# Kernel tuning notes

Measured on AMD Instinct MI355X. Metric: run time of the kernel, lower is better.

Reference implementation:

```python
import jax, jax.numpy as jnp
import numpy as np

N_NODES = 100000
N_EDGES = 1600000
F_IN, NH1, NH2, NH3, N_CLS = 128, 64, 18, 9, 10
KS = [8, 6, 4, 4]
BN_EPS = 1e-5


def setup_inputs() -> dict:
    key = jax.random.key(0)
    ks = jax.random.split(key, 32)
    inp = {
        "x": jax.random.normal(ks[0], (N_NODES, F_IN), dtype=jnp.float32),
        "edge_index": jax.random.randint(ks[1], (2, N_EDGES), 0, N_NODES, dtype=jnp.int32),
    }
    dims = [(F_IN, NH1), (NH1, NH2), (NH2, NH3), (NH3, N_CLS)]
    for i, ((din, dout), K) in enumerate(zip(dims, KS), start=1):
        scale = 1.0 / np.sqrt(din * K)
        inp[f"W{i}"] = jax.random.normal(ks[2 * i], (K, din, dout), dtype=jnp.float32) * scale
        inp[f"b{i}"] = jnp.zeros((dout,), dtype=jnp.float32)
    for i, d in enumerate([NH1, NH2, NH3], start=1):
        inp[f"bn{i}_g"] = jnp.ones((d,), dtype=jnp.float32)
        inp[f"bn{i}_b"] = jnp.zeros((d,), dtype=jnp.float32)
        inp[f"bn{i}_m"] = jnp.zeros((d,), dtype=jnp.float32)
        inp[f"bn{i}_v"] = jnp.ones((d,), dtype=jnp.float32)
    return inp


def _cheb_conv(x, W, b, src, dst, w_norm, n_nodes):
    # PyG ChebConv with lambda_max=2: L_hat = -D^{-1/2} A D^{-1/2}
    def prop(t):  # L_hat @ t via edge scatter
        return jax.ops.segment_sum(w_norm[:, None] * t[src], dst, num_segments=n_nodes)

    K = W.shape[0]
    Tx0 = x
    out = Tx0 @ W[0]
    Tx1 = prop(Tx0)
    out = out + Tx1 @ W[1]
    for k in range(2, K):
        Tx2 = 2.0 * prop(Tx1) - Tx0
        out = out + Tx2 @ W[k]
        Tx0, Tx1 = Tx1, Tx2
    return out + b


def _bn_eval(x, g, b, m, v):
    return (x - m) * (g * jax.lax.rsqrt(v + BN_EPS)) + b


def reference(x, edge_index, W1, b1, W2, b2, W3, b3, W4, b4,
              bn1_g, bn1_b, bn1_m, bn1_v,
              bn2_g, bn2_b, bn2_m, bn2_v,
              bn3_g, bn3_b, bn3_m, bn3_v):
    n = x.shape[0]
    src, dst = edge_index[0], edge_index[1]
    ones = jnp.ones((src.shape[0],), dtype=x.dtype)
    deg = jax.ops.segment_sum(ones, dst, num_segments=n)
    dinv = jnp.where(deg > 0, jax.lax.rsqrt(jnp.maximum(deg, 1.0)), 0.0)
    w_norm = -dinv[src] * dinv[dst]

    h = jax.nn.relu(_bn_eval(_cheb_conv(x, W1, b1, src, dst, w_norm, n), bn1_g, bn1_b, bn1_m, bn1_v))
    h = jax.nn.relu(_bn_eval(_cheb_conv(h, W2, b2, src, dst, w_norm, n), bn2_g, bn2_b, bn2_m, bn2_v))
    h = jax.nn.relu(_bn_eval(_cheb_conv(h, W3, b3, src, dst, w_norm, n), bn3_g, bn3_b, bn3_m, bn3_v))
    return _cheb_conv(h, W4, b4, src, dst, w_norm, n)
```

## Files before the change

kernel.cpp:

```cpp
#include <hip/hip_runtime.h>

#define NN 100000
#define NE 1600000
#define BN_EPS 1e-5f

#define BSH 7
#define BSZ (1 << BSH)
#define NBUCK 782
#define NC 192
#define CE 8334

typedef _Float16 half1;
typedef _Float16 half4 __attribute__((ext_vector_type(4)));
typedef _Float16 h8 __attribute__((ext_vector_type(8)));
typedef float f4 __attribute__((ext_vector_type(4)));
typedef float f8 __attribute__((ext_vector_type(8)));

static inline int divup(int a, int b) { return (a + b - 1) / b; }

__device__ __forceinline__ float wsrc(unsigned int q) {
    unsigned int dg = q >> 17;
    return dg ? rsqrtf((float)dg) : 0.f;
}


__global__ void histb_kernel(const int* __restrict__ dst, int* __restrict__ hist_g) {
    __shared__ int h[NBUCK];
    int c = blockIdx.x;
    for (int i = threadIdx.x; i < NBUCK; i += blockDim.x) h[i] = 0;
    __syncthreads();
    int e0 = c * CE, e1 = min(e0 + CE, NE);
    for (int e = e0 + threadIdx.x; e < e1; e += blockDim.x)
        atomicAdd(&h[dst[e] >> BSH], 1);
    __syncthreads();
    for (int i = threadIdx.x; i < NBUCK; i += blockDim.x) hist_g[c * NBUCK + i] = h[i];
}

__global__ void bscan1_kernel(const int* __restrict__ hist_g, int* __restrict__ bucket_start,
                              int* __restrict__ row_ptr) {
    __shared__ int sh[1024];
    int t = threadIdx.x;
    int tot = 0;
    if (t < NBUCK)
        for (int c = 0; c < NC; ++c) tot += hist_g[c * NBUCK + t];
    sh[t] = (t < NBUCK) ? tot : 0;
    __syncthreads();
    for (int off = 1; off < 1024; off <<= 1) {
        int v = (t >= off) ? sh[t - off] : 0;
        __syncthreads();
        sh[t] += v;
        __syncthreads();
    }
    if (t < NBUCK) bucket_start[t] = sh[t] - tot;
    if (t == 0) { bucket_start[NBUCK] = NE; row_ptr[NN] = NE; }
}

__global__ void boff_kernel(const int* __restrict__ bucket_start, const int* __restrict__ hist_g,
                            int* __restrict__ off_g) {
    int b = blockIdx.x * blockDim.x + threadIdx.x;
    if (b >= NBUCK) return;
    int run = bucket_start[b];
#pragma unroll 4
    for (int c = 0; c < NC; ++c) {
        off_g[c * NBUCK + b] = run;
        run += hist_g[c * NBUCK + b];
    }
}

__global__ void binscatter_kernel(const int* __restrict__ src, const int* __restrict__ dst,
                                  const int* __restrict__ off_g, unsigned int* __restrict__ tmp) {
    __shared__ int off_l[NBUCK];
    int myx = blockIdx.x & 7;
    int c = blockIdx.x >> 3;
    for (int i = threadIdx.x; i < NBUCK; i += blockDim.x)
        off_l[i] = ((i & 7) == myx) ? off_g[c * NBUCK + i] : 0;
    __syncthreads();
    int e0 = c * CE, e1 = min(e0 + CE, NE);
    for (int e = e0 + threadIdx.x; e < e1; e += blockDim.x) {
        int d = dst[e];
        int b = d >> BSH;
        if ((b & 7) != myx) continue;
        int s = src[e];
        int pos = atomicAdd(&off_l[b], 1);
        tmp[pos] = (unsigned int)s | ((unsigned int)(d & (BSZ - 1)) << 25);
    }
}

__global__ void finalize_kernel(const unsigned int* __restrict__ tmp,
                                const int* __restrict__ bucket_start,
                                int* __restrict__ row_ptr, int* __restrict__ deg,
                                unsigned int* __restrict__ cw) {
    __shared__ int cnt[BSZ], sc[BSZ], cur[BSZ];
    int b = blockIdx.x, t = threadIdx.x;
    int e0 = bucket_start[b], e1 = bucket_start[b + 1];
    if (t < BSZ) cnt[t] = 0;
    __syncthreads();
    for (int e = e0 + t; e < e1; e += blockDim.x) atomicAdd(&cnt[tmp[e] >> 25], 1);
    __syncthreads();
    if (t < BSZ) sc[t] = cnt[t];
    __syncthreads();
    for (int off = 1; off < BSZ; off <<= 1) {
        int v = (t >= off && t < BSZ) ? sc[t - off] : 0;
        __syncthreads();
        if (t < BSZ) sc[t] += v;
        __syncthreads();
    }
    if (t < BSZ) {
        int p = e0 + sc[t] - cnt[t];
        cur[t] = p;
        int nd = (b << BSH) + t;
        if (nd < NN) { row_ptr[nd] = p; deg[nd] = cnt[t]; }
    }
    __syncthreads();
    for (int e = e0 + t; e < e1; e += blockDim.x) {
        unsigned int r = tmp[e];
        int ld = r >> 25;
        int k = atomicAdd(&cur[ld], 1);
        cw[k] = r & 0x1FFFFu;
    }
}

__global__ void packdeg_kernel(unsigned int* __restrict__ cw, const int* __restrict__ deg) {
    int e = blockIdx.x * blockDim.x + threadIdx.x;
    if (e >= NE) return;
    unsigned int q = cw[e];
    int dg = deg[q];
    if (dg > 32767) dg = 32767;
    cw[e] = q | ((unsigned int)dg << 17);
}


__global__ void cvtx_kernel(const float4* __restrict__ X, half4* __restrict__ Xh, int tot4) {
    int i = blockIdx.x * blockDim.x + threadIdx.x;
    if (i >= tot4) return;
    float4 v = X[i];
    half4 h;
    h.x = (half1)v.x; h.y = (half1)v.y; h.z = (half1)v.z; h.w = (half1)v.w;
    Xh[i] = h;
}

__global__ void transw_kernel(const float* __restrict__ W, half1* __restrict__ Wt) {
    int i = blockIdx.x * blockDim.x + threadIdx.x;
    if (i >= 512 * 128) return;
    int kd = i >> 9;
    int og = i & 511;
    int k = og >> 6, o = og & 63;
    Wt[(size_t)og * 128 + kd] = (half1)W[((size_t)k * 128 + kd) * 64 + o];
}

__global__ void padw_kernel(const float* __restrict__ src, float* __restrict__ dst,
                            int K, int dins, int douts, int dind, int doutd) {
    int i = blockIdx.x * blockDim.x + threadIdx.x;
    int tot = K * dind * doutd;
    if (i >= tot) return;
    int o = i % doutd;
    int r = i / doutd;
    int dd = r % dind;
    int k = r / dind;
    dst[i] = (dd < dins && o < douts) ? src[((size_t)k * dins + dd) * douts + o] : 0.f;
}

__global__ void proph8_kernel(const h8* __restrict__ feat, const h8* __restrict__ sub,
                              const h8* __restrict__ add, h8* __restrict__ outh,
                              f8* __restrict__ outf,
                              const int* __restrict__ row_ptr, const unsigned int* __restrict__ cw,
                              int n, float scale, int has_sub, int bnrelu,
                              const float* __restrict__ bn_g, const float* __restrict__ bn_b,
                              const float* __restrict__ bn_m, const float* __restrict__ bn_v) {
    int idx = blockIdx.x * blockDim.x + threadIdx.x;
    if (idx >= n * 8) return;
    int nd = idx >> 3;
    int f = idx & 7;
    int e0 = row_ptr[nd], e1 = row_ptr[nd + 1];
    f8 a0 = {0.f, 0.f, 0.f, 0.f, 0.f, 0.f, 0.f, 0.f}, a1 = a0, a2 = a0, a3 = a0;
    int e = e0;
    for (; e + 8 <= e1; e += 8) {
        unsigned int q0 = cw[e], q1 = cw[e + 1], q2 = cw[e + 2], q3 = cw[e + 3];
        unsigned int q4 = cw[e + 4], q5 = cw[e + 5], q6 = cw[e + 6], q7 = cw[e + 7];
        f8 v0 = __builtin_convertvector(feat[(size_t)(q0 & 0x1FFFFu) * 8 + f], f8);
        f8 v1 = __builtin_convertvector(feat[(size_t)(q1 & 0x1FFFFu) * 8 + f], f8);
        f8 v2 = __builtin_convertvector(feat[(size_t)(q2 & 0x1FFFFu) * 8 + f], f8);
        f8 v3 = __builtin_convertvector(feat[(size_t)(q3 & 0x1FFFFu) * 8 + f], f8);
        f8 v4 = __builtin_convertvector(feat[(size_t)(q4 & 0x1FFFFu) * 8 + f], f8);
        f8 v5 = __builtin_convertvector(feat[(size_t)(q5 & 0x1FFFFu) * 8 + f], f8);
        f8 v6 = __builtin_convertvector(feat[(size_t)(q6 & 0x1FFFFu) * 8 + f], f8);
        f8 v7 = __builtin_convertvector(feat[(size_t)(q7 & 0x1FFFFu) * 8 + f], f8);
        a0 += wsrc(q0) * v0;
        a1 += wsrc(q1) * v1;
        a2 += wsrc(q2) * v2;
        a3 += wsrc(q3) * v3;
        a0 += wsrc(q4) * v4;
        a1 += wsrc(q5) * v5;
        a2 += wsrc(q6) * v6;
        a3 += wsrc(q7) * v7;
    }
    for (; e + 4 <= e1; e += 4) {
        unsigned int q0 = cw[e], q1 = cw[e + 1], q2 = cw[e + 2], q3 = cw[e + 3];
        f8 v0 = __builtin_convertvector(feat[(size_t)(q0 & 0x1FFFFu) * 8 + f], f8);
        f8 v1 = __builtin_convertvector(feat[(size_t)(q1 & 0x1FFFFu) * 8 + f], f8);
        f8 v2 = __builtin_convertvector(feat[(size_t)(q2 & 0x1FFFFu) * 8 + f], f8);
        f8 v3 = __builtin_convertvector(feat[(size_t)(q3 & 0x1FFFFu) * 8 + f], f8);
        a0 += wsrc(q0) * v0;
        a1 += wsrc(q1) * v1;
        a2 += wsrc(q2) * v2;
        a3 += wsrc(q3) * v3;
    }
    for (; e < e1; ++e) {
        unsigned int q = cw[e];
        a0 += wsrc(q) * __builtin_convertvector(feat[(size_t)(q & 0x1FFFFu) * 8 + f], f8);
    }
    int degd = e1 - e0;
    float ms = (degd > 0) ? -scale * rsqrtf((float)degd) : 0.f;
    f8 r = ((a0 + a1) + (a2 + a3)) * ms;
    if (has_sub) r -= __builtin_convertvector(sub[idx], f8);
    r += __builtin_convertvector(__builtin_nontemporal_load(&add[idx]), f8);
    if (bnrelu) {
#pragma unroll
        for (int c = 0; c < 8; ++c) {
            int o = f * 8 + c;
            float sc = bn_g[o] * rsqrtf(bn_v[o] + BN_EPS);
            r[c] = fmaxf(fmaf(r[c] - bn_m[o], sc, bn_b[o]), 0.f);
        }
    }
    if (outf) {
        outf[idx] = r;
    } else {
        outh[idx] = __builtin_convertvector(r, h8);
    }
}

__global__ void proph_kernel(const half4* __restrict__ feat, const half4* __restrict__ sub,
                             const half4* __restrict__ add, half4* __restrict__ outh,
                             f4* __restrict__ outf,
                             const int* __restrict__ row_ptr, const unsigned int* __restrict__ cw,
                             int n, int dim4, float scale, int has_sub,
                             int bnrelu, int used,
                             const float* __restrict__ bn_g, const float* __restrict__ bn_b,
                             const float* __restrict__ bn_m, const float* __restrict__ bn_v) {
    int idx = blockIdx.x * blockDim.x + threadIdx.x;
    if (idx >= n * dim4) return;
    int nd = idx / dim4;
    int f = idx - nd * dim4;
    int e0 = row_ptr[nd], e1 = row_ptr[nd + 1];
    f4 a0 = {0.f, 0.f, 0.f, 0.f}, a1 = a0, a2 = a0, a3 = a0;
    int e = e0;
    for (; e + 4 <= e1; e += 4) {
        unsigned int q0 = cw[e], q1 = cw[e + 1], q2 = cw[e + 2], q3 = cw[e + 3];
        f4 v0 = __builtin_convertvector(feat[(size_t)(q0 & 0x1FFFFu) * dim4 + f], f4);
        f4 v1 = __builtin_convertvector(feat[(size_t)(q1 & 0x1FFFFu) * dim4 + f], f4);
        f4 v2 = __builtin_convertvector(feat[(size_t)(q2 & 0x1FFFFu) * dim4 + f], f4);
        f4 v3 = __builtin_convertvector(feat[(size_t)(q3 & 0x1FFFFu) * dim4 + f], f4);
        a0 += wsrc(q0) * v0;
        a1 += wsrc(q1) * v1;
        a2 += wsrc(q2) * v2;
        a3 += wsrc(q3) * v3;
    }
    for (; e < e1; ++e) {
        unsigned int q = cw[e];
        a0 += wsrc(q) * __builtin_convertvector(feat[(size_t)(q & 0x1FFFFu) * dim4 + f], f4);
    }
    int degd = e1 - e0;
    float ms = (degd > 0) ? -scale * rsqrtf((float)degd) : 0.f;
    f4 r = ((a0 + a1) + (a2 + a3)) * ms;
    if (has_sub) r -= __builtin_convertvector(sub[idx], f4);
    r += __builtin_convertvector(__builtin_nontemporal_load(&add[idx]), f4);
    if (bnrelu) {
#pragma unroll
        for (int c = 0; c < 4; ++c) {
            int o = f * 4 + c;
            if (o < used) {
                float sc = bn_g[o] * rsqrtf(bn_v[o] + BN_EPS);
                r[c] = fmaxf(fmaf(r[c] - bn_m[o], sc, bn_b[o]), 0.f);
            } else r[c] = 0.f;
        }
    }
    if (outf) {
        outf[idx] = r;
    } else {
        half4 h;
        h.x = (half1)r.x; h.y = (half1)r.y; h.z = (half1)r.z; h.w = (half1)r.w;
        outh[idx] = h;
    }
}

__global__ void propl_kernel(const half4* __restrict__ feat, const half4* __restrict__ sub,
                             const half4* __restrict__ add, float* __restrict__ out,
                             const int* __restrict__ row_ptr, const unsigned int* __restrict__ cw,
                             int n) {
    int idx = blockIdx.x * blockDim.x + threadIdx.x;
    if (idx >= n * 3) return;
    int nd = idx / 3;
    int f = idx - nd * 3;
    int e0 = row_ptr[nd], e1 = row_ptr[nd + 1];
    f4 a0 = {0.f, 0.f, 0.f, 0.f}, a1 = a0, a2 = a0, a3 = a0;
    int e = e0;
    for (; e + 4 <= e1; e += 4) {
        unsigned int q0 = cw[e], q1 = cw[e + 1], q2 = cw[e + 2], q3 = cw[e + 3];
        a0 += wsrc(q0) * __builtin_convertvector(feat[(size_t)(q0 & 0x1FFFFu) * 3 + f], f4);
        a1 += wsrc(q1) * __builtin_convertvector(feat[(size_t)(q1 & 0x1FFFFu) * 3 + f], f4);
        a2 += wsrc(q2) * __builtin_convertvector(feat[(size_t)(q2 & 0x1FFFFu) * 3 + f], f4);
        a3 += wsrc(q3) * __builtin_convertvector(feat[(size_t)(q3 & 0x1FFFFu) * 3 + f], f4);
    }
    for (; e < e1; ++e) {
        unsigned int q = cw[e];
        a0 += wsrc(q) * __builtin_convertvector(feat[(size_t)(q & 0x1FFFFu) * 3 + f], f4);
    }
    int degd = e1 - e0;
    float ms = (degd > 0) ? -rsqrtf((float)degd) : 0.f;
    f4 r = ((a0 + a1) + (a2 + a3)) * ms;
    r -= __builtin_convertvector(sub[idx], f4);
    r += __builtin_convertvector(add[idx], f4);
    int o = f * 4;
    float* orow = out + (size_t)nd * 10;
    if (o + 0 < 10) orow[o + 0] = r.x;
    if (o + 1 < 10) orow[o + 1] = r.y;
    if (o + 2 < 10) orow[o + 2] = r.z;
    if (o + 3 < 10) orow[o + 3] = r.w;
}

#define LSTR 68
__global__ __launch_bounds__(512) void gemm_mfma_kernel(
        const half1* __restrict__ Xh, const half1* __restrict__ Wt,
        const float* __restrict__ bias, half1* __restrict__ CB, int n) {
    __shared__ half1 lds[8 * 32 * LSTR];
    int lane = threadIdx.x & 63;
    int ks = threadIdx.x >> 6;
    int m16 = lane & 15;
    int quad = lane >> 4;
    int ntile = blockIdx.x * 64;

    f4 acc[4][4];
#pragma unroll
    for (int nt = 0; nt < 4; ++nt)
#pragma unroll
        for (int i = 0; i < 4; ++i) acc[nt][i] = (f4){0.f, 0.f, 0.f, 0.f};

#pragma unroll
    for (int kc = 0; kc < 4; ++kc) {
        int koff = kc * 32 + quad * 8;
        h8 a[4];
#pragma unroll
        for (int i = 0; i < 4; ++i)
            a[i] = *(const h8*)(Wt + (size_t)(ks * 64 + i * 16 + m16) * 128 + koff);
        h8 b[4];
#pragma unroll
        for (int nt = 0; nt < 4; ++nt) {
            int node = min(ntile + nt * 16 + m16, n - 1);
            b[nt] = *(const h8*)(Xh + (size_t)node * 128 + koff);
        }
#pragma unroll
        for (int nt = 0; nt < 4; ++nt)
#pragma unroll
            for (int i = 0; i < 4; ++i)
                acc[nt][i] = __builtin_amdgcn_mfma_f32_16x16x32_f16(a[i], b[nt], acc[nt][i], 0, 0, 0);
    }

    half1* slab = lds + (size_t)ks * 32 * LSTR;
    int nl0 = lane >> 3;
    int chunk = lane & 7;
#pragma unroll
    for (int hh = 0; hh < 2; ++hh) {
#pragma unroll
        for (int p = 0; p < 2; ++p) {
            int nt = hh * 2 + p;
            int node_l = p * 16 + m16;
#pragma unroll
            for (int i = 0; i < 4; ++i) {
                int ob = i * 16 + quad * 4;
                f4 v = acc[nt][i];
                if (ks == 0) {
                    const f4 b4 = *(const f4*)(bias + ob);
                    v += b4;
                }
                half4 h;
                h.x = (half1)v[0]; h.y = (half1)v[1]; h.z = (half1)v[2]; h.w = (half1)v[3];
                *(half4*)(slab + node_l * LSTR + ob) = h;
            }
        }
        asm volatile("s_waitcnt lgkmcnt(0)" ::: "memory");
#pragma unroll
        for (int j = 0; j < 4; ++j) {
            int node_l = j * 8 + nl0;
            int node = ntile + hh * 32 + node_l;
            if (node < n) {
                h8 v = *(const h8*)(slab + node_l * LSTR + chunk * 8);
                *(h8*)(CB + ((size_t)ks * n + node) * 64 + chunk * 8) = v;
            }
        }
    }
}

template <int KK, int DIN4, int NACC>
__global__ void gemm_smallw_kernel(const float* __restrict__ X, const float* __restrict__ Wp,
                                   const float* __restrict__ bias, int dout,
                                   half4* __restrict__ CB, int n) {
    int lane = threadIdx.x & 63;
    int k = __builtin_amdgcn_readfirstlane((int)(threadIdx.x >> 6));
    int node0 = blockIdx.x * 64 + lane;
    int node = min(node0, n - 1);
    f4 acc[NACC];
#pragma unroll
    for (int i = 0; i < NACC; ++i) {
        f4 v = {0.f, 0.f, 0.f, 0.f};
        if (k == 0 && bias) {
#pragma unroll
            for (int c = 0; c < 4; ++c) {
                int o = i * 4 + c;
                v[c] = (o < dout) ? bias[o] : 0.f;
            }
        }
        acc[i] = v;
    }
    const f4* Xr = (const f4*)(X + (size_t)node * (DIN4 * 4));
    const f4* Wk = (const f4*)(Wp + (size_t)k * (DIN4 * 4) * (NACC * 4));
    for (int d4 = 0; d4 < DIN4; ++d4) {
        f4 xv = Xr[d4];
#pragma unroll
        for (int j = 0; j < 4; ++j) {
            float xs = xv[j];
#pragma unroll
            for (int i = 0; i < NACC; ++i)
                acc[i] += xs * Wk[(d4 * 4 + j) * NACC + i];
        }
    }
    if (node0 < n) {
        size_t base = ((size_t)k * n + node) * NACC;
#pragma unroll
        for (int i = 0; i < NACC; ++i) {
            half4 h;
            h.x = (half1)acc[i].x; h.y = (half1)acc[i].y;
            h.z = (half1)acc[i].z; h.w = (half1)acc[i].w;
            CB[base + i] = h;
        }
    }
}


extern "C" void kernel_launch(void* const* d_in, const int* in_sizes, int n_in,
                              void* d_out, int out_size, void* d_ws, size_t ws_size,
                              hipStream_t stream) {
    const float* x  = (const float*)d_in[0];
    const int*   ei = (const int*)d_in[1];
    const float* Wl[4] = {(const float*)d_in[2], (const float*)d_in[4],
                          (const float*)d_in[6], (const float*)d_in[8]};
    const float* bl[4] = {(const float*)d_in[3], (const float*)d_in[5],
                          (const float*)d_in[7], (const float*)d_in[9]};
    const float* bn[3][4];
    for (int l = 0; l < 3; ++l)
        for (int j = 0; j < 4; ++j)
            bn[l][j] = (const float*)d_in[10 + 4 * l + j];

    char* ws = (char*)d_ws;
    size_t off = 0;
    auto alloc = [&](size_t bytes) -> void* {
        void* p = (void*)(ws + off);
        off = (off + bytes + 255) & ~(size_t)255;
        return p;
    };
    int*   deg      = (int*)alloc(NN * 4);
    int*   row_ptr  = (int*)alloc((NN + 1) * 4);
    int*   bstart   = (int*)alloc((NBUCK + 1) * 4);
    unsigned int* cw = (unsigned int*)alloc((size_t)NE * 4);
    half1* CB1h    = (half1*)alloc((size_t)8 * NN * 64 * 2);
    half1* CBsh    = (half1*)alloc((size_t)6 * NN * 20 * 2);
    half1* S0      = (half1*)alloc((size_t)NN * 64 * 2);
    half1* S1      = (half1*)alloc((size_t)NN * 64 * 2);
    half1* S2      = (half1*)alloc((size_t)NN * 64 * 2);
    float* H1f     = (float*)alloc((size_t)NN * 64 * 4);
    float* H2f     = (float*)alloc((size_t)NN * 20 * 4);
    float* H3f     = (float*)alloc((size_t)NN * 12 * 4);
    float* Wp2     = (float*)alloc((size_t)6 * 64 * 20 * 4);
    float* Wp3     = (float*)alloc((size_t)4 * 20 * 12 * 4);
    float* Wp4     = (float*)alloc((size_t)4 * 12 * 12 * 4);
    half1* Xh      = (half1*)alloc((size_t)NN * 128 * 2);
    half1* Wt1     = (half1*)alloc((size_t)512 * 128 * 2);

    unsigned int* tmp = (unsigned int*)CB1h;
    int* hist_g = (int*)((char*)CB1h + (16u << 20));
    int* off_g  = hist_g + NC * NBUCK;

    const int* srcp = ei;
    const int* dstp = ei + NE;
    const int NB = divup(NN, 64);

    histb_kernel<<<NC, 256, 0, stream>>>(dstp, hist_g);
    bscan1_kernel<<<1, 1024, 0, stream>>>(hist_g, bstart, row_ptr);
    boff_kernel<<<divup(NBUCK, 256), 256, 0, stream>>>(bstart, hist_g, off_g);
    binscatter_kernel<<<NC * 8, 256, 0, stream>>>(srcp, dstp, off_g, tmp);
    finalize_kernel<<<NBUCK, 256, 0, stream>>>(tmp, bstart, row_ptr, deg, cw);
    packdeg_kernel<<<divup(NE, 256), 256, 0, stream>>>(cw, deg);

    cvtx_kernel<<<divup(NN * 32, 256), 256, 0, stream>>>((const float4*)x, (half4*)Xh, NN * 32);
    transw_kernel<<<divup(512 * 128, 256), 256, 0, stream>>>(Wl[0], Wt1);
    padw_kernel<<<divup(6 * 64 * 20, 256), 256, 0, stream>>>(Wl[1], Wp2, 6, 64, 18, 64, 20);
    padw_kernel<<<divup(4 * 20 * 12, 256), 256, 0, stream>>>(Wl[2], Wp3, 4, 18, 9, 20, 12);
    padw_kernel<<<divup(4 * 12 * 12, 256), 256, 0, stream>>>(Wl[3], Wp4, 4, 9, 10, 12, 12);

    auto prop1 = [&](const half1* feat, const half1* sub, const half1* add,
                     half1* outh, float* outf, float scale, int bnrelu,
                     const float* g, const float* bb, const float* m, const float* v) {
        proph8_kernel<<<divup(NN * 8, 256), 256, 0, stream>>>(
            (const h8*)feat, (const h8*)sub, (const h8*)add,
            (h8*)outh, (f8*)outf, row_ptr, cw, NN, scale,
            sub != nullptr, bnrelu, g, bb, m, v);
    };
    auto prop = [&](const half1* feat, const half1* sub, const half1* add,
                    half1* outh, float* outf, int dim4, float scale,
                    int bnrelu, int used, const float* g, const float* bb,
                    const float* m, const float* v) {
        proph_kernel<<<divup(NN * dim4, 256), 256, 0, stream>>>(
            (const half4*)feat, (const half4*)sub, (const half4*)add,
            (half4*)outh, (f4*)outf, row_ptr, cw, NN, dim4, scale,
            sub != nullptr, bnrelu, used, g, bb, m, v);
    };

    gemm_mfma_kernel<<<NB, 512, 0, stream>>>(Xh, Wt1, bl[0], CB1h, NN);
    {
        auto C = [&](int k) { return (const half1*)(CB1h + (size_t)k * NN * 64); };
        prop1(C(7), nullptr, C(6), S0, nullptr, 2.f, 0, 0, 0, 0, 0);
        prop1(S0, C(7), C(5), S1, nullptr, 2.f, 0, 0, 0, 0, 0);
        prop1(S1, S0, C(4), S2, nullptr, 2.f, 0, 0, 0, 0, 0);
        prop1(S2, S1, C(3), S0, nullptr, 2.f, 0, 0, 0, 0, 0);
        prop1(S0, S2, C(2), S1, nullptr, 2.f, 0, 0, 0, 0, 0);
        prop1(S1, S0, C(1), S2, nullptr, 2.f, 0, 0, 0, 0, 0);
        prop1(S2, S1, C(0), nullptr, H1f, 1.f, 1,
              bn[0][0], bn[0][1], bn[0][2], bn[0][3]);
    }

    gemm_smallw_kernel<6, 16, 5><<<NB, 384, 0, stream>>>(H1f, Wp2, bl[1], 18,
                                                         (half4*)CBsh, NN);
    {
        auto C = [&](int k) { return (const half1*)(CBsh + (size_t)k * NN * 20); };
        prop(C(5), nullptr, C(4), S0, nullptr, 5, 2.f, 0, 18, 0, 0, 0, 0);
        prop(S0, C(5), C(3), S1, nullptr, 5, 2.f, 0, 18, 0, 0, 0, 0);
        prop(S1, S0, C(2), S2, nullptr, 5, 2.f, 0, 18, 0, 0, 0, 0);
        prop(S2, S1, C(1), S0, nullptr, 5, 2.f, 0, 18, 0, 0, 0, 0);
        prop(S0, S2, C(0), nullptr, H2f, 5, 1.f, 1, 18,
             bn[1][0], bn[1][1], bn[1][2], bn[1][3]);
    }

    gemm_smallw_kernel<4, 5, 3><<<NB, 256, 0, stream>>>(H2f, Wp3, bl[2], 9,
                                                        (half4*)CBsh, NN);
    {
        auto C = [&](int k) { return (const half1*)(CBsh + (size_t)k * NN * 12); };
        prop(C(3), nullptr, C(2), S0, nullptr, 3, 2.f, 0, 9, 0, 0, 0, 0);
        prop(S0, C(3), C(1), S1, nullptr, 3, 2.f, 0, 9, 0, 0, 0, 0);
        prop(S1, S0, C(0), nullptr, H3f, 3, 1.f, 1, 9,
             bn[2][0], bn[2][1], bn[2][2], bn[2][3]);
    }

    gemm_smallw_kernel<4, 3, 3><<<NB, 256, 0, stream>>>(H3f, Wp4, bl[3], 10,
                                                        (half4*)CBsh, NN);
    {
        auto C = [&](int k) { return (const half1*)(CBsh + (size_t)k * NN * 12); };
        prop(C(3), nullptr, C(2), S0, nullptr, 3, 2.f, 0, 10, 0, 0, 0, 0);
        prop(S0, C(3), C(1), S1, nullptr, 3, 2.f, 0, 10, 0, 0, 0, 0);
        propl_kernel<<<divup(NN * 3, 256), 256, 0, stream>>>(
            (const half4*)S1, (const half4*)S0, (const half4*)CBsh,
            (float*)d_out, row_ptr, cw, NN);
    }
}
```

Measured before the change: 795.1 us.

## Sort nodes by degree for load-balanced propagation and halve GEMM node tile

Adds a counting sort of nodes by in-degree (histogram, scan, rank kernels) and makes every propagation kernel process nodes in that order, so threads in a wavefront have similar edge-loop lengths and divergence drops. Output, sub and add accesses become indirect through the permutation, which loses coalescing on those streams and drops the nontemporal load hint. Separately, the first-layer MFMA GEMM tile shrinks from 64 to 32 nodes per block, doubling the block count and simplifying the LDS write-out.

```diff
diff --git a/kernel.cpp b/kernel.cpp
--- a/kernel.cpp
+++ b/kernel.cpp
@@ -127,6 +127,54 @@
     int dg = deg[q];
     if (dg > 32767) dg = 32767;
     cw[e] = q | ((unsigned int)dg << 17);
+}
+
+
+__global__ void histdeg_kernel(const int* __restrict__ deg, int* __restrict__ dbin, int n) {
+    __shared__ int lh[128];
+    int t = threadIdx.x;
+    if (t < 128) lh[t] = 0;
+    __syncthreads();
+    for (int i = blockIdx.x * blockDim.x + t; i < n; i += gridDim.x * blockDim.x)
+        atomicAdd(&lh[min(deg[i], 127)], 1);
+    __syncthreads();
+    if (t < 128 && lh[t]) atomicAdd(&dbin[t], lh[t]);
+}
+
+__global__ void scanbin_kernel(int* __restrict__ dbin) {
+    __shared__ int sh[128];
+    int t = threadIdx.x;
+    int own = dbin[t];
+    sh[t] = own;
+    __syncthreads();
+    for (int off = 1; off < 128; off <<= 1) {
+        int v = (t >= off) ? sh[t - off] : 0;
+        __syncthreads();
+        sh[t] += v;
+        __syncthreads();
+    }
+    dbin[t] = sh[t] - own;
+}
+
+__global__ void rank_kernel(const int* __restrict__ deg, int* __restrict__ dbin,
+                            int* __restrict__ order, int n) {
+    __shared__ int lh[128], lbase[128], lcur[128];
+    int t = threadIdx.x;
+    if (t < 128) lh[t] = 0;
+    __syncthreads();
+    int i = blockIdx.x * blockDim.x + t;
+    int b = -1;
+    if (i < n) { b = min(deg[i], 127); atomicAdd(&lh[b], 1); }
+    __syncthreads();
+    if (t < 128) {
+        lcur[t] = 0;
+        lbase[t] = lh[t] ? atomicAdd(&dbin[t], lh[t]) : 0;
+    }
+    __syncthreads();
+    if (i < n) {
+        int off = atomicAdd(&lcur[b], 1);
+        order[lbase[b] + off] = i;
+    }
 }
 
 
@@ -164,13 +212,15 @@
                               const h8* __restrict__ add, h8* __restrict__ outh,
                               f8* __restrict__ outf,
                               const int* __restrict__ row_ptr, const unsigned int* __restrict__ cw,
+                              const int* __restrict__ order,
                               int n, float scale, int has_sub, int bnrelu,
                               const float* __restrict__ bn_g, const float* __restrict__ bn_b,
                               const float* __restrict__ bn_m, const float* __restrict__ bn_v) {
     int idx = blockIdx.x * blockDim.x + threadIdx.x;
     if (idx >= n * 8) return;
-    int nd = idx >> 3;
+    int nd = order[idx >> 3];
     int f = idx & 7;
+    int m = nd * 8 + f;
     int e0 = row_ptr[nd], e1 = row_ptr[nd + 1];
     f8 a0 = {0.f, 0.f, 0.f, 0.f, 0.f, 0.f, 0.f, 0.f}, a1 = a0, a2 = a0, a3 = a0;
     int e = e0;
@@ -212,8 +262,8 @@
     int degd = e1 - e0;
     float ms = (degd > 0) ? -scale * rsqrtf((float)degd) : 0.f;
     f8 r = ((a0 + a1) + (a2 + a3)) * ms;
-    if (has_sub) r -= __builtin_convertvector(sub[idx], f8);
-    r += __builtin_convertvector(__builtin_nontemporal_load(&add[idx]), f8);
+    if (has_sub) r -= __builtin_convertvector(sub[m], f8);
+    r += __builtin_convertvector(add[m], f8);
     if (bnrelu) {
 #pragma unroll
         for (int c = 0; c < 8; ++c) {
@@ -223,9 +273,9 @@
         }
     }
     if (outf) {
-        outf[idx] = r;
+        outf[m] = r;
     } else {
-        outh[idx] = __builtin_convertvector(r, h8);
+        outh[m] = __builtin_convertvector(r, h8);
     }
 }
 
@@ -233,14 +283,17 @@
                              const half4* __restrict__ add, half4* __restrict__ outh,
                              f4* __restrict__ outf,
                              const int* __restrict__ row_ptr, const unsigned int* __restrict__ cw,
+                             const int* __restrict__ order,
                              int n, int dim4, float scale, int has_sub,
                              int bnrelu, int used,
                              const float* __restrict__ bn_g, const float* __restrict__ bn_b,
                              const float* __restrict__ bn_m, const float* __restrict__ bn_v) {
     int idx = blockIdx.x * blockDim.x + threadIdx.x;
     if (idx >= n * dim4) return;
-    int nd = idx / dim4;
-    int f = idx - nd * dim4;
+    int grp = idx / dim4;
+    int f = idx - grp * dim4;
+    int nd = order[grp];
+    int m = nd * dim4 + f;
     int e0 = row_ptr[nd], e1 = row_ptr[nd + 1];
     f4 a0 = {0.f, 0.f, 0.f, 0.f}, a1 = a0, a2 = a0, a3 = a0;
     int e = e0;
@@ -262,8 +315,8 @@
     int degd = e1 - e0;
     float ms = (degd > 0) ? -scale * rsqrtf((float)degd) : 0.f;
     f4 r = ((a0 + a1) + (a2 + a3)) * ms;
-    if (has_sub) r -= __builtin_convertvector(sub[idx], f4);
-    r += __builtin_convertvector(__builtin_nontemporal_load(&add[idx]), f4);
+    if (has_sub) r -= __builtin_convertvector(sub[m], f4);
+    r += __builtin_convertvector(add[m], f4);
     if (bnrelu) {
 #pragma unroll
         for (int c = 0; c < 4; ++c) {
@@ -275,22 +328,24 @@
         }
     }
     if (outf) {
-        outf[idx] = r;
+        outf[m] = r;
     } else {
         half4 h;
         h.x = (half1)r.x; h.y = (half1)r.y; h.z = (half1)r.z; h.w = (half1)r.w;
-        outh[idx] = h;
+        outh[m] = h;
     }
 }
 
 __global__ void propl_kernel(const half4* __restrict__ feat, const half4* __restrict__ sub,
                              const half4* __restrict__ add, float* __restrict__ out,
                              const int* __restrict__ row_ptr, const unsigned int* __restrict__ cw,
-                             int n) {
+                             const int* __restrict__ order, int n) {
     int idx = blockIdx.x * blockDim.x + threadIdx.x;
     if (idx >= n * 3) return;
-    int nd = idx / 3;
-    int f = idx - nd * 3;
+    int grp = idx / 3;
+    int f = idx - grp * 3;
+    int nd = order[grp];
+    int m = nd * 3 + f;
     int e0 = row_ptr[nd], e1 = row_ptr[nd + 1];
     f4 a0 = {0.f, 0.f, 0.f, 0.f}, a1 = a0, a2 = a0, a3 = a0;
     int e = e0;
@@ -308,8 +363,8 @@
     int degd = e1 - e0;
     float ms = (degd > 0) ? -rsqrtf((float)degd) : 0.f;
     f4 r = ((a0 + a1) + (a2 + a3)) * ms;
-    r -= __builtin_convertvector(sub[idx], f4);
-    r += __builtin_convertvector(add[idx], f4);
+    r -= __builtin_convertvector(sub[m], f4);
+    r += __builtin_convertvector(add[m], f4);
     int o = f * 4;
     float* orow = out + (size_t)nd * 10;
     if (o + 0 < 10) orow[o + 0] = r.x;
@@ -327,11 +382,11 @@
     int ks = threadIdx.x >> 6;
     int m16 = lane & 15;
     int quad = lane >> 4;
-    int ntile = blockIdx.x * 64;
-
-    f4 acc[4][4];
-#pragma unroll
-    for (int nt = 0; nt < 4; ++nt)
+    int ntile = blockIdx.x * 32;
+
+    f4 acc[2][4];
+#pragma unroll
+    for (int nt = 0; nt < 2; ++nt)
 #pragma unroll
         for (int i = 0; i < 4; ++i) acc[nt][i] = (f4){0.f, 0.f, 0.f, 0.f};
 
@@ -342,50 +397,46 @@
 #pragma unroll
         for (int i = 0; i < 4; ++i)
             a[i] = *(const h8*)(Wt + (size_t)(ks * 64 + i * 16 + m16) * 128 + koff);
-        h8 b[4];
-#pragma unroll
-        for (int nt = 0; nt < 4; ++nt) {
+        h8 b[2];
+#pragma unroll
+        for (int nt = 0; nt < 2; ++nt) {
             int node = min(ntile + nt * 16 + m16, n - 1);
             b[nt] = *(const h8*)(Xh + (size_t)node * 128 + koff);
         }
 #pragma unroll
-        for (int nt = 0; nt < 4; ++nt)
+        for (int nt = 0; nt < 2; ++nt)
 #pragma unroll
             for (int i = 0; i < 4; ++i)
                 acc[nt][i] = __builtin_amdgcn_mfma_f32_16x16x32_f16(a[i], b[nt], acc[nt][i], 0, 0, 0);
     }
 
     half1* slab = lds + (size_t)ks * 32 * LSTR;
+#pragma unroll
+    for (int nt = 0; nt < 2; ++nt) {
+        int node_l = nt * 16 + m16;
+#pragma unroll
+        for (int i = 0; i < 4; ++i) {
+            int ob = i * 16 + quad * 4;
+            f4 v = acc[nt][i];
+            if (ks == 0) {
+                const f4 b4 = *(const f4*)(bias + ob);
+                v += b4;
+            }
+            half4 h;
+            h.x = (half1)v[0]; h.y = (half1)v[1]; h.z = (half1)v[2]; h.w = (half1)v[3];
+            *(half4*)(slab + node_l * LSTR + ob) = h;
+        }
+    }
+    asm volatile("s_waitcnt lgkmcnt(0)" ::: "memory");
     int nl0 = lane >> 3;
     int chunk = lane & 7;
 #pragma unroll
-    for (int hh = 0; hh < 2; ++hh) {
-#pragma unroll
-        for (int p = 0; p < 2; ++p) {
-            int nt = hh * 2 + p;
-            int node_l = p * 16 + m16;
-#pragma unroll
-            for (int i = 0; i < 4; ++i) {
-                int ob = i * 16 + quad * 4;
-                f4 v = acc[nt][i];
-                if (ks == 0) {
-                    const f4 b4 = *(const f4*)(bias + ob);
-                    v += b4;
-                }
-                half4 h;
-                h.x = (half1)v[0]; h.y = (half1)v[1]; h.z = (half1)v[2]; h.w = (half1)v[3];
-                *(half4*)(slab + node_l * LSTR + ob) = h;
-            }
-        }
-        asm volatile("s_waitcnt lgkmcnt(0)" ::: "memory");
-#pragma unroll
-        for (int j = 0; j < 4; ++j) {
-            int node_l = j * 8 + nl0;
-            int node = ntile + hh * 32 + node_l;
-            if (node < n) {
-                h8 v = *(const h8*)(slab + node_l * LSTR + chunk * 8);
-                *(h8*)(CB + ((size_t)ks * n + node) * 64 + chunk * 8) = v;
-            }
+    for (int j = 0; j < 4; ++j) {
+        int node_l = j * 8 + nl0;
+        int node = ntile + node_l;
+        if (node < n) {
+            h8 v = *(const h8*)(slab + node_l * LSTR + chunk * 8);
+            *(h8*)(CB + ((size_t)ks * n + node) * 64 + chunk * 8) = v;
         }
     }
 }
@@ -460,6 +511,8 @@
     int*   deg      = (int*)alloc(NN * 4);
     int*   row_ptr  = (int*)alloc((NN + 1) * 4);
     int*   bstart   = (int*)alloc((NBUCK + 1) * 4);
+    int*   order    = (int*)alloc(NN * 4);
+    int*   dbin     = (int*)alloc(128 * 4);
     unsigned int* cw = (unsigned int*)alloc((size_t)NE * 4);
     half1* CB1h    = (half1*)alloc((size_t)8 * NN * 64 * 2);
     half1* CBsh    = (half1*)alloc((size_t)6 * NN * 20 * 2);
@@ -482,12 +535,17 @@
     const int* srcp = ei;
     const int* dstp = ei + NE;
     const int NB = divup(NN, 64);
-
+    const int NB32 = divup(NN, 32);
+
+    hipMemsetAsync(dbin, 0, 128 * 4, stream);
     histb_kernel<<<NC, 256, 0, stream>>>(dstp, hist_g);
     bscan1_kernel<<<1, 1024, 0, stream>>>(hist_g, bstart, row_ptr);
     boff_kernel<<<divup(NBUCK, 256), 256, 0, stream>>>(bstart, hist_g, off_g);
     binscatter_kernel<<<NC * 8, 256, 0, stream>>>(srcp, dstp, off_g, tmp);
     finalize_kernel<<<NBUCK, 256, 0, stream>>>(tmp, bstart, row_ptr, deg, cw);
+    histdeg_kernel<<<64, 256, 0, stream>>>(deg, dbin, NN);
+    scanbin_kernel<<<1, 128, 0, stream>>>(dbin);
+    rank_kernel<<<divup(NN, 256), 256, 0, stream>>>(deg, dbin, order, NN);
     packdeg_kernel<<<divup(NE, 256), 256, 0, stream>>>(cw, deg);
 
     cvtx_kernel<<<divup(NN * 32, 256), 256, 0, stream>>>((const float4*)x, (half4*)Xh, NN * 32);
@@ -501,7 +559,7 @@
                      const float* g, const float* bb, const float* m, const float* v) {
         proph8_kernel<<<divup(NN * 8, 256), 256, 0, stream>>>(
             (const h8*)feat, (const h8*)sub, (const h8*)add,
-            (h8*)outh, (f8*)outf, row_ptr, cw, NN, scale,
+            (h8*)outh, (f8*)outf, row_ptr, cw, order, NN, scale,
             sub != nullptr, bnrelu, g, bb, m, v);
     };
     auto prop = [&](const half1* feat, const half1* sub, const half1* add,
@@ -510,11 +568,11 @@
                     const float* m, const float* v) {
         proph_kernel<<<divup(NN * dim4, 256), 256, 0, stream>>>(
             (const half4*)feat, (const half4*)sub, (const half4*)add,
-            (half4*)outh, (f4*)outf, row_ptr, cw, NN, dim4, scale,
+            (half4*)outh, (f4*)outf, row_ptr, cw, order, NN, dim4, scale,
             sub != nullptr, bnrelu, used, g, bb, m, v);
     };
 
-    gemm_mfma_kernel<<<NB, 512, 0, stream>>>(Xh, Wt1, bl[0], CB1h, NN);
+    gemm_mfma_kernel<<<NB32, 512, 0, stream>>>(Xh, Wt1, bl[0], CB1h, NN);
     {
         auto C = [&](int k) { return (const half1*)(CB1h + (size_t)k * NN * 64); };
         prop1(C(7), nullptr, C(6), S0, nullptr, 2.f, 0, 0, 0, 0, 0);
@@ -557,6 +615,6 @@
         prop(S0, C(3), C(1), S1, nullptr, 3, 2.f, 0, 10, 0, 0, 0, 0);
         propl_kernel<<<divup(NN * 3, 256), 256, 0, stream>>>(
             (const half4*)S1, (const half4*)S0, (const half4*)CBsh,
-            (float*)d_out, row_ptr, cw, NN);
-    }
-}
+            (float*)d_out, row_ptr, cw, order, NN);
+    }
+}
```

Measured after the change: 891.4 us. 12.1% more time.

## Split layer-1 features into 16-wide quarter slabs and propagate each separately

Applied to the files above, without the earlier changes.

The first-layer GEMM output is now stored as four quarter-width slabs, each holding 16 features per node for all nodes, instead of one 64-wide row per node. Propagation launches four kernels, one per slab, with 2 threads per node. Each gather then touches a 3.2 MB working set that fits better in L2/MALL, instead of the full 12.8 MB array. The cost is reading the edge list four times, plus four times the launches; edge-index loads are also marked nontemporal.

```diff
diff --git a/kernel.cpp b/kernel.cpp
--- a/kernel.cpp
+++ b/kernel.cpp
@@ -160,72 +160,55 @@
     dst[i] = (dd < dins && o < douts) ? src[((size_t)k * dins + dd) * douts + o] : 0.f;
 }
 
-__global__ void proph8_kernel(const h8* __restrict__ feat, const h8* __restrict__ sub,
-                              const h8* __restrict__ add, h8* __restrict__ outh,
-                              f8* __restrict__ outf,
+__global__ void prophq_kernel(const h8* __restrict__ featq, const h8* __restrict__ subq,
+                              const h8* __restrict__ addq, h8* __restrict__ outhq,
+                              f8* __restrict__ outfq,
                               const int* __restrict__ row_ptr, const unsigned int* __restrict__ cw,
                               int n, float scale, int has_sub, int bnrelu,
                               const float* __restrict__ bn_g, const float* __restrict__ bn_b,
                               const float* __restrict__ bn_m, const float* __restrict__ bn_v) {
     int idx = blockIdx.x * blockDim.x + threadIdx.x;
-    if (idx >= n * 8) return;
-    int nd = idx >> 3;
-    int f = idx & 7;
+    if (idx >= n * 2) return;
+    int nd = idx >> 1;
+    int j = idx & 1;
     int e0 = row_ptr[nd], e1 = row_ptr[nd + 1];
     f8 a0 = {0.f, 0.f, 0.f, 0.f, 0.f, 0.f, 0.f, 0.f}, a1 = a0, a2 = a0, a3 = a0;
     int e = e0;
-    for (; e + 8 <= e1; e += 8) {
-        unsigned int q0 = cw[e], q1 = cw[e + 1], q2 = cw[e + 2], q3 = cw[e + 3];
-        unsigned int q4 = cw[e + 4], q5 = cw[e + 5], q6 = cw[e + 6], q7 = cw[e + 7];
-        f8 v0 = __builtin_convertvector(feat[(size_t)(q0 & 0x1FFFFu) * 8 + f], f8);
-        f8 v1 = __builtin_convertvector(feat[(size_t)(q1 & 0x1FFFFu) * 8 + f], f8);
-        f8 v2 = __builtin_convertvector(feat[(size_t)(q2 & 0x1FFFFu) * 8 + f], f8);
-        f8 v3 = __builtin_convertvector(feat[(size_t)(q3 & 0x1FFFFu) * 8 + f], f8);
-        f8 v4 = __builtin_convertvector(feat[(size_t)(q4 & 0x1FFFFu) * 8 + f], f8);
-        f8 v5 = __builtin_convertvector(feat[(size_t)(q5 & 0x1FFFFu) * 8 + f], f8);
-        f8 v6 = __builtin_convertvector(feat[(size_t)(q6 & 0x1FFFFu) * 8 + f], f8);
-        f8 v7 = __builtin_convertvector(feat[(size_t)(q7 & 0x1FFFFu) * 8 + f], f8);
+    for (; e + 4 <= e1; e += 4) {
+        unsigned int q0 = __builtin_nontemporal_load(&cw[e]);
+        unsigned int q1 = __builtin_nontemporal_load(&cw[e + 1]);
+        unsigned int q2 = __builtin_nontemporal_load(&cw[e + 2]);
+        unsigned int q3 = __builtin_nontemporal_load(&cw[e + 3]);
+        f8 v0 = __builtin_convertvector(featq[(size_t)(q0 & 0x1FFFFu) * 2 + j], f8);
+        f8 v1 = __builtin_convertvector(featq[(size_t)(q1 & 0x1FFFFu) * 2 + j], f8);
+        f8 v2 = __builtin_convertvector(featq[(size_t)(q2 & 0x1FFFFu) * 2 + j], f8);
+        f8 v3 = __builtin_convertvector(featq[(size_t)(q3 & 0x1FFFFu) * 2 + j], f8);
         a0 += wsrc(q0) * v0;
         a1 += wsrc(q1) * v1;
         a2 += wsrc(q2) * v2;
         a3 += wsrc(q3) * v3;
-        a0 += wsrc(q4) * v4;
-        a1 += wsrc(q5) * v5;
-        a2 += wsrc(q6) * v6;
-        a3 += wsrc(q7) * v7;
-    }
-    for (; e + 4 <= e1; e += 4) {
-        unsigned int q0 = cw[e], q1 = cw[e + 1], q2 = cw[e + 2], q3 = cw[e + 3];
-        f8 v0 = __builtin_convertvector(feat[(size_t)(q0 & 0x1FFFFu) * 8 + f], f8);
-        f8 v1 = __builtin_convertvector(feat[(size_t)(q1 & 0x1FFFFu) * 8 + f], f8);
-        f8 v2 = __builtin_convertvector(feat[(size_t)(q2 & 0x1FFFFu) * 8 + f], f8);
-        f8 v3 = __builtin_convertvector(feat[(size_t)(q3 & 0x1FFFFu) * 8 + f], f8);
-        a0 += wsrc(q0) * v0;
-        a1 += wsrc(q1) * v1;
-        a2 += wsrc(q2) * v2;
-        a3 += wsrc(q3) * v3;
     }
     for (; e < e1; ++e) {
         unsigned int q = cw[e];
-        a0 += wsrc(q) * __builtin_convertvector(feat[(size_t)(q & 0x1FFFFu) * 8 + f], f8);
+        a0 += wsrc(q) * __builtin_convertvector(featq[(size_t)(q & 0x1FFFFu) * 2 + j], f8);
     }
     int degd = e1 - e0;
     float ms = (degd > 0) ? -scale * rsqrtf((float)degd) : 0.f;
     f8 r = ((a0 + a1) + (a2 + a3)) * ms;
-    if (has_sub) r -= __builtin_convertvector(sub[idx], f8);
-    r += __builtin_convertvector(__builtin_nontemporal_load(&add[idx]), f8);
+    if (has_sub) r -= __builtin_convertvector(__builtin_nontemporal_load(&subq[idx]), f8);
+    r += __builtin_convertvector(__builtin_nontemporal_load(&addq[idx]), f8);
     if (bnrelu) {
 #pragma unroll
         for (int c = 0; c < 8; ++c) {
-            int o = f * 8 + c;
+            int o = j * 8 + c;
             float sc = bn_g[o] * rsqrtf(bn_v[o] + BN_EPS);
             r[c] = fmaxf(fmaf(r[c] - bn_m[o], sc, bn_b[o]), 0.f);
         }
     }
-    if (outf) {
-        outf[idx] = r;
+    if (outfq) {
+        outfq[(size_t)nd * 8 + j] = r;
     } else {
-        outh[idx] = __builtin_convertvector(r, h8);
+        outhq[idx] = __builtin_convertvector(r, h8);
     }
 }
 
@@ -356,8 +339,8 @@
     }
 
     half1* slab = lds + (size_t)ks * 32 * LSTR;
-    int nl0 = lane >> 3;
-    int chunk = lane & 7;
+    int nl = lane >> 1;
+    int jh = lane & 1;
 #pragma unroll
     for (int hh = 0; hh < 2; ++hh) {
 #pragma unroll
@@ -379,12 +362,11 @@
         }
         asm volatile("s_waitcnt lgkmcnt(0)" ::: "memory");
 #pragma unroll
-        for (int j = 0; j < 4; ++j) {
-            int node_l = j * 8 + nl0;
-            int node = ntile + hh * 32 + node_l;
+        for (int q = 0; q < 4; ++q) {
+            int node = ntile + hh * 32 + nl;
             if (node < n) {
-                h8 v = *(const h8*)(slab + node_l * LSTR + chunk * 8);
-                *(h8*)(CB + ((size_t)ks * n + node) * 64 + chunk * 8) = v;
+                h8 v = *(const h8*)(slab + nl * LSTR + q * 16 + jh * 8);
+                *((h8*)CB + ((size_t)(ks * 4 + q) * n + node) * 2 + jh) = v;
             }
         }
     }
@@ -499,10 +481,18 @@
     auto prop1 = [&](const half1* feat, const half1* sub, const half1* add,
                      half1* outh, float* outf, float scale, int bnrelu,
                      const float* g, const float* bb, const float* m, const float* v) {
-        proph8_kernel<<<divup(NN * 8, 256), 256, 0, stream>>>(
-            (const h8*)feat, (const h8*)sub, (const h8*)add,
-            (h8*)outh, (f8*)outf, row_ptr, cw, NN, scale,
-            sub != nullptr, bnrelu, g, bb, m, v);
+        for (int q = 0; q < 4; ++q) {
+            const h8* fq = (const h8*)feat + (size_t)q * NN * 2;
+            const h8* sq = sub ? (const h8*)sub + (size_t)q * NN * 2 : nullptr;
+            const h8* aq = (const h8*)add + (size_t)q * NN * 2;
+            h8* oq = outh ? (h8*)outh + (size_t)q * NN * 2 : nullptr;
+            f8* ofq = outf ? (f8*)outf + q * 2 : nullptr;
+            prophq_kernel<<<divup(NN * 2, 256), 256, 0, stream>>>(
+                fq, sq, aq, oq, ofq, row_ptr, cw, NN, scale,
+                sub != nullptr, bnrelu,
+                g ? g + 16 * q : nullptr, bb ? bb + 16 * q : nullptr,
+                m ? m + 16 * q : nullptr, v ? v + 16 * q : nullptr);
+        }
     };
     auto prop = [&](const half1* feat, const half1* sub, const half1* add,
                     half1* outh, float* outf, int dim4, float scale,
```

Result: slower. 1.132 ms (+42.3%).
